# Kernel optimization log

Hardware: AMD Instinct MI355X
Metric: run time of the kernel (lower is better)

The kernel has to match this reference:

```python
import jax, jax.numpy as jnp
import numpy as np

L = 4          # num_layers
D = 512        # gconv_dim == tlayer_dim
HG, CG = 8, 64 # gconv heads, head dim (D//8)
HT, CT = 4, 128  # tlayer heads, head dim
FF = 4 * D
G, NPG = 128, 256
N = G * NPG
E = N * 16
AF, AV = 9, 64   # atom features / vocab
BF, BV = 3, 8    # bond features / vocab
OUT = 128
SCALE = 0.02


def setup_inputs() -> dict:
    key = jax.random.key(0)
    ks = iter(jax.random.split(key, 64))
    rn = lambda shape: (jax.random.normal(next(ks), shape, dtype=jnp.float32) * SCALE)
    inp = {}
    # float params (stacked over layers)
    inp['atom_emb'] = rn((AF, AV, D))
    inp['bond_emb'] = rn((BF, BV, D))
    for nm in ['gq_w', 'gk_w', 'gv_w', 'ge_w', 'gskip_w', 'mid_w']:
        inp[nm] = rn((L, D, D))
    for nm in ['gq_b', 'gk_b', 'gv_b', 'gskip_b', 'mid_b']:
        inp[nm] = rn((L, D))
    inp['mid_g'] = jnp.ones((L, D), jnp.float32)
    inp['mid_bt'] = jnp.zeros((L, D), jnp.float32)
    for nm in ['tq_w', 'tk_w', 'tv_w', 'to_w']:
        inp[nm] = rn((L, D, D))
    for nm in ['tq_b', 'tk_b', 'tv_b', 'to_b']:
        inp[nm] = rn((L, D))
    inp['ln1_g'] = jnp.ones((L, D), jnp.float32)
    inp['ln1_b'] = jnp.zeros((L, D), jnp.float32)
    inp['f1_w'] = rn((L, D, FF))
    inp['f1_b'] = rn((L, FF))
    inp['f2_w'] = rn((L, FF, D))
    inp['f2_b'] = rn((L, D))
    inp['ln2_g'] = jnp.ones((L, D), jnp.float32)
    inp['ln2_b'] = jnp.zeros((L, D), jnp.float32)
    inp['out_w'] = rn((D, OUT))
    inp['out_b'] = rn((OUT,))
    # int inputs
    inp['x'] = jax.random.randint(next(ks), (N, AF), 0, AV, dtype=jnp.int32)
    inp['edge_attr'] = jax.random.randint(next(ks), (E, BF), 0, BV, dtype=jnp.int32)
    # intra-graph edges: random offsets within each graph
    gid = jax.random.randint(next(ks), (E,), 0, G, dtype=jnp.int32)
    src = gid * NPG + jax.random.randint(next(ks), (E,), 0, NPG, dtype=jnp.int32)
    dst = gid * NPG + jax.random.randint(next(ks), (E,), 0, NPG, dtype=jnp.int32)
    inp['edge_index'] = jnp.stack([src, dst])
    inp['batch'] = jnp.repeat(jnp.arange(G, dtype=jnp.int32), NPG)
    return inp


def _ln(x, g, b, eps=1e-5):
    mu = x.mean(-1, keepdims=True)
    var = ((x - mu) ** 2).mean(-1, keepdims=True)
    return (x - mu) * jax.lax.rsqrt(var + eps) * g + b


def _forward(atom_emb, bond_emb, gq_w, gq_b, gk_w, gk_b, gv_w, gv_b, ge_w,
             gskip_w, gskip_b, mid_w, mid_b, mid_g, mid_bt,
             tq_w, tq_b, tk_w, tk_b, tv_w, tv_b, to_w, to_b,
             ln1_g, ln1_b, f1_w, f1_b, f2_w, f2_b, ln2_g, ln2_b,
             out_w, out_b, x, edge_index, edge_attr, batch):
    # encoders: sum of per-feature embeddings (OGB AtomEncoder/BondEncoder)
    h = atom_emb[jnp.arange(AF)[None, :], x].sum(1)          # [N, D]
    e_attr = bond_emb[jnp.arange(BF)[None, :], edge_attr].sum(1)  # [E, D]
    src, dst = edge_index[0], edge_index[1]

    for i in range(L):
        # --- TransformerConv (PyG): edge-conditioned multi-head graph attention
        q = (h @ gq_w[i] + gq_b[i]).reshape(N, HG, CG)
        k = (h @ gk_w[i] + gk_b[i]).reshape(N, HG, CG)
        v = (h @ gv_w[i] + gv_b[i]).reshape(N, HG, CG)
        ee = (e_attr @ ge_w[i]).reshape(E, HG, CG)           # lin_edge (no bias)
        ke = k[src] + ee
        ve = v[src] + ee
        logits = (q[dst] * ke).sum(-1) / np.sqrt(CG)          # [E, HG]
        m = jax.ops.segment_max(logits, dst, num_segments=N)
        p = jnp.exp(logits - m[dst])
        denom = jax.ops.segment_sum(p, dst, num_segments=N) + 1e-16
        alpha = p / denom[dst]
        agg = jax.ops.segment_sum(alpha[..., None] * ve, dst, num_segments=N)
        h = agg.reshape(N, D) + h @ gskip_w[i] + gskip_b[i]   # root skip
        # --- middle Linear + LayerNorm + ReLU
        h = jax.nn.relu(_ln(h @ mid_w[i] + mid_b[i], mid_g[i], mid_bt[i]))

    xg = h.reshape(G, NPG, D)
    for i in range(L):
        # --- transformer encoder layer, dense attention within each graph
        q = (xg @ tq_w[i] + tq_b[i]).reshape(G, NPG, HT, CT)
        k = (xg @ tk_w[i] + tk_b[i]).reshape(G, NPG, HT, CT)
        v = (xg @ tv_w[i] + tv_b[i]).reshape(G, NPG, HT, CT)
        attn = jax.nn.softmax(jnp.einsum('gqhc,gkhc->ghqk', q, k) / np.sqrt(CT), axis=-1)
        o = jnp.einsum('ghqk,gkhc->gqhc', attn, v).reshape(G, NPG, D)
        xg = _ln(xg + (o @ to_w[i] + to_b[i]), ln1_g[i], ln1_b[i])
        ff = jax.nn.relu(xg @ f1_w[i] + f1_b[i]) @ f2_w[i] + f2_b[i]
        xg = _ln(xg + ff, ln2_g[i], ln2_b[i])

    # mean readout over nodes per graph (segment mean via batch)
    hflat = xg.reshape(N, D)
    cnt = jax.ops.segment_sum(jnp.ones((N,), hflat.dtype), batch, num_segments=G)
    pooled = jax.ops.segment_sum(hflat, batch, num_segments=G) / cnt[:, None]
    return pooled @ out_w + out_b                              # [G, OUT]


def reference(atom_emb, bond_emb, gq_w, gq_b, gk_w, gk_b, gv_w, gv_b, ge_w,
              gskip_w, gskip_b, mid_w, mid_b, mid_g, mid_bt,
              tq_w, tq_b, tk_w, tk_b, tv_w, tv_b, to_w, to_b,
              ln1_g, ln1_b, f1_w, f1_b, f2_w, f2_b, ln2_g, ln2_b,
              out_w, out_b, x, edge_index, edge_attr, batch):
    return _forward(atom_emb, bond_emb, gq_w, gq_b, gk_w, gk_b, gv_w, gv_b, ge_w,
                    gskip_w, gskip_b, mid_w, mid_b, mid_g, mid_bt,
                    tq_w, tq_b, tk_w, tk_b, tv_w, tv_b, to_w, to_b,
                    ln1_g, ln1_b, f1_w, f1_b, f2_w, f2_b, ln2_g, ln2_b,
                    out_w, out_b, x, edge_index, edge_attr, batch)
```

## Files before the change

### kernel.cpp

```cpp
#include <hip/hip_runtime.h>
#include <hip/hip_bf16.h>
#include <math.h>

#define N_NODES 32768
#define DIM     512
#define NE      524288
#define NL      4
#define NG      128
#define NPG_    256
#define HG_     8
#define CG_     64
#define HT_     4
#define CT_     128
#define FF_     2048
#define AF_     9
#define AV_     64
#define BV_     8
#define OUTD    128

typedef unsigned short u16;
typedef __attribute__((ext_vector_type(8))) short bhalf8;
typedef __attribute__((ext_vector_type(4))) float floatx4;
typedef __attribute__((ext_vector_type(8))) unsigned short u16x8;
typedef __attribute__((ext_vector_type(4))) unsigned short u16x4;

__device__ __forceinline__ u16 f2bf(float f) {
  union { float f; unsigned u; } x; x.f = f;
  unsigned r = x.u + 0x7fffu + ((x.u >> 16) & 1u);
  return (u16)(r >> 16);
}
__device__ __forceinline__ float bf2f(u16 u) {
  union { unsigned u; float f; } x; x.u = ((unsigned)u) << 16; return x.f;
}

#define GL2LDS(gp, lp) __builtin_amdgcn_global_load_lds( \
    (const __attribute__((address_space(1))) unsigned int*)(gp), \
    (__attribute__((address_space(3))) unsigned int*)(lp), 16, 0, 0)

__global__ __launch_bounds__(128) void atom_enc_kernel(
    const float* __restrict__ emb, const int* __restrict__ x, u16* __restrict__ hb) {
  int n = blockIdx.x;
  int d4 = threadIdx.x;
  const int* xr = x + n * AF_;
  float4 acc = {0.f, 0.f, 0.f, 0.f};
#pragma unroll
  for (int f = 0; f < AF_; ++f) {
    int idx = xr[f];
    const float4 v = *(const float4*)&emb[((size_t)(f * AV_ + idx)) * DIM + 4 * d4];
    acc.x += v.x; acc.y += v.y; acc.z += v.z; acc.w += v.w;
  }
  u16x4 o;
  o[0] = f2bf(acc.x); o[1] = f2bf(acc.y); o[2] = f2bf(acc.z); o[3] = f2bf(acc.w);
  *(u16x4*)&hb[(size_t)n * DIM + 4 * d4] = o;
}

__global__ __launch_bounds__(512) void bemb_proj_kernel(
    const float* __restrict__ bond_emb, const float* __restrict__ gew, u16* __restrict__ tab) {
  int r = blockIdx.x;
  int d = threadIdx.x;
  const float* a = bond_emb + (size_t)r * DIM;
  float acc = 0.f;
#pragma unroll 8
  for (int kx = 0; kx < DIM; ++kx) acc += a[kx] * gew[(size_t)kx * DIM + d];
  tab[(size_t)r * DIM + d] = f2bf(acc);
}

__global__ __launch_bounds__(256) void wcvt_kernel(
    const float* __restrict__ W, u16* __restrict__ Wt, int K, int N) {
  __shared__ float t[32][33];
  const size_t mo = (size_t)blockIdx.z * K * N;
  int k0 = blockIdx.y * 32, n0 = blockIdx.x * 32;
  int tx = threadIdx.x & 31, ty = threadIdx.x >> 5;
#pragma unroll
  for (int i = 0; i < 32; i += 8)
    t[ty + i][tx] = W[mo + (size_t)(k0 + ty + i) * N + n0 + tx];
  __syncthreads();
#pragma unroll
  for (int i = 0; i < 32; i += 8)
    Wt[mo + (size_t)(n0 + ty + i) * K + k0 + tx] = f2bf(t[tx][ty + i]);
}

__global__ __launch_bounds__(256) void gemm_mfma_kernel(
    const u16* __restrict__ A, const u16* __restrict__ Bt,
    const float* __restrict__ bias, float* __restrict__ Cf, u16* __restrict__ Cb,
    int K, int Nout, int relu, int bf16out, int vtout) {
  __shared__ __align__(16) u16 As[4096];
  __shared__ __align__(16) u16 Bs[4096];
  const int tid = threadIdx.x;
  const int wave = tid >> 6, lane = tid & 63;
  const int bm = blockIdx.y * 128, bn = blockIdx.x * 128;
  const int wr = wave >> 1, wc = wave & 1;

  const size_t rowA = (size_t)bm + (tid >> 2);
  const size_t rowB = (size_t)bn + (tid >> 2);
  const int gofs = (tid & 3) * 8;
  const u16* pA = A + rowA * K + gofs;
  const u16* pB = Bt + rowB * K + gofs;
  u16* lA0 = &As[wave * 512];
  u16* lB0 = &Bs[wave * 512];
  const size_t skip64 = (size_t)64 * K;

  floatx4 acc[4][4] = {};
  const int r = lane & 15, kg = lane >> 4;
  const int aoff = (wr * 64 + r) * 32 + kg * 8;
  const int boff = (wc * 64 + r) * 32 + kg * 8;

  for (int k0 = 0; k0 < K; k0 += 32) {
    GL2LDS(pA + k0, lA0);
    GL2LDS(pA + skip64 + k0, lA0 + 2048);
    GL2LDS(pB + k0, lB0);
    GL2LDS(pB + skip64 + k0, lB0 + 2048);
    __syncthreads();
    bhalf8 af[4], bg[4];
#pragma unroll
    for (int mi = 0; mi < 4; ++mi) af[mi] = *(const bhalf8*)&As[aoff + mi * 512];
#pragma unroll
    for (int ni = 0; ni < 4; ++ni) bg[ni] = *(const bhalf8*)&Bs[boff + ni * 512];
#pragma unroll
    for (int mi = 0; mi < 4; ++mi)
#pragma unroll
      for (int ni = 0; ni < 4; ++ni)
        acc[mi][ni] = __builtin_amdgcn_mfma_f32_16x16x32_bf16(af[mi], bg[ni], acc[mi][ni], 0, 0, 0);
    __syncthreads();
  }

  const int rb = (lane >> 4) * 4;
  const int cc = lane & 15;
#pragma unroll
  for (int mi = 0; mi < 4; ++mi) {
#pragma unroll
    for (int ni = 0; ni < 4; ++ni) {
      int gr0 = bm + wr * 64 + mi * 16 + rb;
      int gc = bn + wc * 64 + ni * 16 + cc;
      float bv = bias[gc];
#pragma unroll
      for (int reg = 0; reg < 4; ++reg) {
        int gr = gr0 + reg;
        float v = acc[mi][ni][reg] + bv;
        if (relu) v = fmaxf(v, 0.f);
        if (vtout)        Cb[((size_t)(gr >> 8) * DIM + gc) * NPG_ + (gr & 255)] = f2bf(v);
        else if (bf16out) Cb[(size_t)gr * Nout + gc] = f2bf(v);
        else              Cf[(size_t)gr * Nout + gc] = v;
      }
    }
  }
}

__global__ __launch_bounds__(256) void attn_s_mfma_kernel(
    const u16* __restrict__ q, const u16* __restrict__ k, u16* __restrict__ S, int zbase) {
  __shared__ __align__(16) u16 As[4096];
  __shared__ __align__(16) u16 Bs[4096];
  const int tid = threadIdx.x;
  const int wave = tid >> 6, lane = tid & 63;
  const int zl = blockIdx.z, z = zbase + zl, g = z >> 2, hh = z & 3;
  const int bm = blockIdx.y * 128, bn = blockIdx.x * 128;
  const int wr = wave >> 1, wc = wave & 1;
  const u16* qg = q + (size_t)g * NPG_ * DIM + hh * CT_;
  const u16* kg2 = k + (size_t)g * NPG_ * DIM + hh * CT_;
  const u16* pA = qg + (size_t)(bm + (tid >> 2)) * DIM + (tid & 3) * 8;
  const u16* pB = kg2 + (size_t)(bn + (tid >> 2)) * DIM + (tid & 3) * 8;
  u16* lA0 = &As[wave * 512];
  u16* lB0 = &Bs[wave * 512];
  const size_t skip64 = (size_t)64 * DIM;
  floatx4 acc[4][4] = {};
  const int r = lane & 15, kg_ = lane >> 4;
  const int aoff = (wr * 64 + r) * 32 + kg_ * 8;
  const int boff = (wc * 64 + r) * 32 + kg_ * 8;
  for (int k0 = 0; k0 < CT_; k0 += 32) {
    GL2LDS(pA + k0, lA0);
    GL2LDS(pA + skip64 + k0, lA0 + 2048);
    GL2LDS(pB + k0, lB0);
    GL2LDS(pB + skip64 + k0, lB0 + 2048);
    __syncthreads();
    bhalf8 af[4], bg[4];
#pragma unroll
    for (int mi = 0; mi < 4; ++mi) af[mi] = *(const bhalf8*)&As[aoff + mi * 512];
#pragma unroll
    for (int ni = 0; ni < 4; ++ni) bg[ni] = *(const bhalf8*)&Bs[boff + ni * 512];
#pragma unroll
    for (int mi = 0; mi < 4; ++mi)
#pragma unroll
      for (int ni = 0; ni < 4; ++ni)
        acc[mi][ni] = __builtin_amdgcn_mfma_f32_16x16x32_bf16(af[mi], bg[ni], acc[mi][ni], 0, 0, 0);
    __syncthreads();
  }
  const float sc = 0.08838834764831845f;
  u16* C = S + (size_t)zl * NPG_ * NPG_;
  const int rb = (lane >> 4) * 4, cc = lane & 15;
#pragma unroll
  for (int mi = 0; mi < 4; ++mi)
#pragma unroll
    for (int ni = 0; ni < 4; ++ni) {
      int gr = bm + wr * 64 + mi * 16 + rb;
      int gc = bn + wc * 64 + ni * 16 + cc;
#pragma unroll
      for (int reg = 0; reg < 4; ++reg)
        C[(size_t)(gr + reg) * NPG_ + gc] = f2bf(acc[mi][ni][reg] * sc);
    }
}

__global__ __launch_bounds__(256) void softmax256_kernel(u16* __restrict__ SP) {
  size_t row = (size_t)blockIdx.x * 4 + (threadIdx.x >> 6);
  int lane = threadIdx.x & 63;
  u16* r = SP + row * NPG_;
  u16x4 v = *(u16x4*)&r[lane * 4];
  float x0 = bf2f(v[0]), x1 = bf2f(v[1]), x2 = bf2f(v[2]), x3 = bf2f(v[3]);
  float m = fmaxf(fmaxf(x0, x1), fmaxf(x2, x3));
#pragma unroll
  for (int off = 32; off; off >>= 1) m = fmaxf(m, __shfl_xor(m, off));
  x0 = expf(x0 - m); x1 = expf(x1 - m); x2 = expf(x2 - m); x3 = expf(x3 - m);
  float s = x0 + x1 + x2 + x3;
#pragma unroll
  for (int off = 32; off; off >>= 1) s += __shfl_xor(s, off);
  float inv = 1.0f / s;
  u16x4 o;
  o[0] = f2bf(x0 * inv); o[1] = f2bf(x1 * inv);
  o[2] = f2bf(x2 * inv); o[3] = f2bf(x3 * inv);
  *(u16x4*)&r[lane * 4] = o;
}

__global__ __launch_bounds__(256) void attn_o_mfma_kernel(
    const u16* __restrict__ P, const u16* __restrict__ vt, u16* __restrict__ O, int zbase) {
  __shared__ __align__(16) u16 As[4096];
  __shared__ __align__(16) u16 Bs[4096];
  const int tid = threadIdx.x;
  const int wave = tid >> 6, lane = tid & 63;
  const int zl = blockIdx.z, z = zbase + zl, g = z >> 2, hh = z & 3;
  const int bm = blockIdx.y * 128;
  const int wr = wave >> 1, wc = wave & 1;
  const u16* A = P + (size_t)zl * NPG_ * NPG_;
  const u16* Bt = vt + ((size_t)g * DIM + hh * CT_) * NPG_;
  const u16* pA = A + (size_t)(bm + (tid >> 2)) * NPG_ + (tid & 3) * 8;
  const u16* pB = Bt + (size_t)(tid >> 2) * NPG_ + (tid & 3) * 8;
  u16* lA0 = &As[wave * 512];
  u16* lB0 = &Bs[wave * 512];
  const size_t skip64 = (size_t)64 * NPG_;
  floatx4 acc[4][4] = {};
  const int r = lane & 15, kg_ = lane >> 4;
  const int aoff = (wr * 64 + r) * 32 + kg_ * 8;
  const int boff = (wc * 64 + r) * 32 + kg_ * 8;
  for (int k0 = 0; k0 < NPG_; k0 += 32) {
    GL2LDS(pA + k0, lA0);
    GL2LDS(pA + skip64 + k0, lA0 + 2048);
    GL2LDS(pB + k0, lB0);
    GL2LDS(pB + skip64 + k0, lB0 + 2048);
    __syncthreads();
    bhalf8 af[4], bg[4];
#pragma unroll
    for (int mi = 0; mi < 4; ++mi) af[mi] = *(const bhalf8*)&As[aoff + mi * 512];
#pragma unroll
    for (int ni = 0; ni < 4; ++ni) bg[ni] = *(const bhalf8*)&Bs[boff + ni * 512];
#pragma unroll
    for (int mi = 0; mi < 4; ++mi)
#pragma unroll
      for (int ni = 0; ni < 4; ++ni)
        acc[mi][ni] = __builtin_amdgcn_mfma_f32_16x16x32_bf16(af[mi], bg[ni], acc[mi][ni], 0, 0, 0);
    __syncthreads();
  }
  u16* C = O + ((size_t)g * NPG_) * DIM + hh * CT_;
  const int rb = (lane >> 4) * 4, cc = lane & 15;
#pragma unroll
  for (int mi = 0; mi < 4; ++mi)
#pragma unroll
    for (int ni = 0; ni < 4; ++ni) {
      int gr = bm + wr * 64 + mi * 16 + rb;
      int gc = wc * 64 + ni * 16 + cc;
#pragma unroll
      for (int reg = 0; reg < 4; ++reg)
        C[(size_t)(gr + reg) * DIM + gc] = f2bf(acc[mi][ni][reg]);
    }
}

__global__ __launch_bounds__(256) void gemm_bias_kernel(
    const float* __restrict__ A, const float* __restrict__ W,
    const float* __restrict__ bias, float* __restrict__ C,
    int M, int K, int Nout, int relu) {
  __shared__ float As[16][65];
  __shared__ float Bs[16][64];
  const int bm = blockIdx.y * 64;
  const int bn = blockIdx.x * 64;
  const int tid = threadIdx.x;
  const int tx = tid & 15, ty = tid >> 4;
  float acc[4][4] = {};
  for (int k0 = 0; k0 < K; k0 += 16) {
    {
      int row = tid >> 2;
      int kq = (tid & 3) << 2;
      float4 a = *(const float4*)&A[(size_t)(bm + row) * K + k0 + kq];
      As[kq + 0][row] = a.x; As[kq + 1][row] = a.y; As[kq + 2][row] = a.z; As[kq + 3][row] = a.w;
    }
    {
      int krow = tid >> 4;
      int cq = (tid & 15) << 2;
      *(float4*)&Bs[krow][cq] = *(const float4*)&W[(size_t)(k0 + krow) * Nout + bn + cq];
    }
    __syncthreads();
#pragma unroll
    for (int kk = 0; kk < 16; ++kk) {
      float a[4];
#pragma unroll
      for (int i = 0; i < 4; ++i) a[i] = As[kk][ty * 4 + i];
      float4 b4 = *(const float4*)&Bs[kk][tx * 4];
      float b[4] = {b4.x, b4.y, b4.z, b4.w};
#pragma unroll
      for (int i = 0; i < 4; ++i)
#pragma unroll
        for (int j = 0; j < 4; ++j) acc[i][j] = fmaf(a[i], b[j], acc[i][j]);
    }
    __syncthreads();
  }
  float4 bv = *(const float4*)&bias[bn + tx * 4];
#pragma unroll
  for (int i = 0; i < 4; ++i) {
    int row = bm + ty * 4 + i;
    float4 o;
    o.x = acc[i][0] + bv.x; o.y = acc[i][1] + bv.y;
    o.z = acc[i][2] + bv.z; o.w = acc[i][3] + bv.w;
    if (relu) {
      o.x = fmaxf(o.x, 0.f); o.y = fmaxf(o.y, 0.f);
      o.z = fmaxf(o.z, 0.f); o.w = fmaxf(o.w, 0.f);
    }
    *(float4*)&C[(size_t)row * Nout + bn + tx * 4] = o;
  }
}

__global__ __launch_bounds__(256) void deg_count_kernel(const int* __restrict__ ei, int* __restrict__ deg) {
  int e = blockIdx.x * 256 + threadIdx.x;
  atomicAdd(&deg[ei[NE + e]], 1);
}

__global__ __launch_bounds__(1024) void scan_kernel(const int* __restrict__ deg, int* __restrict__ rp) {
  __shared__ int sums[1024];
  int t = threadIdx.x;
  int base = t * 32;
  int local[32];
  int s = 0;
#pragma unroll
  for (int i = 0; i < 32; ++i) { local[i] = s; s += deg[base + i]; }
  sums[t] = s;
  __syncthreads();
  for (int off = 1; off < 1024; off <<= 1) {
    int other = (t >= off) ? sums[t - off] : 0;
    __syncthreads();
    sums[t] += other;
    __syncthreads();
  }
  int chunk_off = sums[t] - s;
#pragma unroll
  for (int i = 0; i < 32; ++i) rp[base + i] = chunk_off + local[i];
  if (t == 1023) rp[N_NODES] = sums[1023];
}

__global__ __launch_bounds__(256) void scatter_kernel(
    const int* __restrict__ ei, const int* __restrict__ rp,
    int* __restrict__ cur, int* __restrict__ csr) {
  int e = blockIdx.x * 256 + threadIdx.x;
  int d = ei[NE + e];
  int pos = atomicAdd(&cur[d], 1);
  csr[rp[d] + pos] = e;
}

__global__ __launch_bounds__(256) void edge_logits_kernel(
    const u16* __restrict__ q, const u16* __restrict__ k, const u16* __restrict__ tab,
    const int* __restrict__ ei, const int* __restrict__ ea, float* __restrict__ logits) {
  int e = blockIdx.x * 4 + (threadIdx.x >> 6);
  int lane = threadIdx.x & 63;
  int src = ei[e], dst = ei[NE + e];
  int a0 = ea[e * 3], a1 = ea[e * 3 + 1], a2 = ea[e * 3 + 2];
  const u16x8 qv = *(const u16x8*)&q[(size_t)dst * DIM + lane * 8];
  const u16x8 kv = *(const u16x8*)&k[(size_t)src * DIM + lane * 8];
  const size_t to = (size_t)lane * 8;
  const u16x8 e0 = *(const u16x8*)&tab[(size_t)a0 * DIM + to];
  const u16x8 e1 = *(const u16x8*)&tab[(size_t)(8 + a1) * DIM + to];
  const u16x8 e2 = *(const u16x8*)&tab[(size_t)(16 + a2) * DIM + to];
  float acc = 0.f;
#pragma unroll
  for (int j = 0; j < 8; ++j) {
    float ee = bf2f(e0[j]) + bf2f(e1[j]) + bf2f(e2[j]);
    acc += bf2f(qv[j]) * (bf2f(kv[j]) + ee);
  }
  acc += __shfl_xor(acc, 1);
  acc += __shfl_xor(acc, 2);
  acc += __shfl_xor(acc, 4);
  if ((lane & 7) == 0) logits[(size_t)e * HG_ + (lane >> 3)] = acc * 0.125f;
}

#define CHUNK 128
__global__ __launch_bounds__(512) void edge_agg_kernel(
    const u16* __restrict__ v, const u16* __restrict__ tab, const float* __restrict__ logits,
    const float* __restrict__ skip, const int* __restrict__ ei, const int* __restrict__ ea,
    const int* __restrict__ rp, const int* __restrict__ csr, u16* __restrict__ hnew) {
  int n = blockIdx.x;
  int d = threadIdx.x;
  int hh = d >> 6;
  int start = rp[n];
  int deg = rp[n + 1] - start;
  __shared__ int s_src[CHUNK];
  __shared__ int s_ea[CHUNK];
  __shared__ int s_eid[CHUNK];
  __shared__ float s_l[CHUNK * HG_];
  float runmax = -3.0e38f, denom = 0.f, accum = 0.f;
  for (int c0 = 0; c0 < deg; c0 += CHUNK) {
    int cnt = min(CHUNK, deg - c0);
    __syncthreads();
    if (d < cnt) {
      int eid = csr[start + c0 + d];
      s_eid[d] = eid;
      s_src[d] = ei[eid];
      s_ea[d] = ea[eid * 3] | (ea[eid * 3 + 1] << 8) | (ea[eid * 3 + 2] << 16);
    }
    __syncthreads();
    for (int j = d; j < cnt * HG_; j += 512)
      s_l[j] = logits[(size_t)s_eid[j >> 3] * HG_ + (j & 7)];
    __syncthreads();
    float cmax = -3.0e38f;
    for (int j = 0; j < cnt; ++j) cmax = fmaxf(cmax, s_l[j * HG_ + hh]);
    float nm = fmaxf(runmax, cmax);
    if (nm > runmax) {
      float rr = expf(runmax - nm);
      denom *= rr; accum *= rr; runmax = nm;
    }
    for (int j = 0; j < cnt; ++j) {
      float p = expf(s_l[j * HG_ + hh] - runmax);
      int srcn = s_src[j];
      int eap = s_ea[j];
      float ee = bf2f(tab[(size_t)(eap & 0xff) * DIM + d])
               + bf2f(tab[(size_t)(8 + ((eap >> 8) & 0xff)) * DIM + d])
               + bf2f(tab[(size_t)(16 + (eap >> 16)) * DIM + d]);
      float ve = bf2f(v[(size_t)srcn * DIM + d]) + ee;
      denom += p;
      accum += p * ve;
    }
  }
  size_t o = (size_t)n * DIM + d;
  hnew[o] = f2bf(accum / (denom + 1e-16f) + skip[o]);
}

__global__ __launch_bounds__(256) void ln_kernel(
    const float* __restrict__ in, const u16* __restrict__ resid,
    const float* __restrict__ g, const float* __restrict__ b,
    u16* __restrict__ outb, int relu) {
  int row = blockIdx.x * 4 + (threadIdx.x >> 6);
  int lane = threadIdx.x & 63;
  size_t base = (size_t)row * DIM + lane * 8;
  float x[8];
  {
    float4 v0 = *(const float4*)&in[base];
    float4 v1 = *(const float4*)&in[base + 4];
    x[0] = v0.x; x[1] = v0.y; x[2] = v0.z; x[3] = v0.w;
    x[4] = v1.x; x[5] = v1.y; x[6] = v1.z; x[7] = v1.w;
  }
  if (resid) {
    u16x8 rv = *(const u16x8*)&resid[base];
#pragma unroll
    for (int i = 0; i < 8; ++i) x[i] += bf2f(rv[i]);
  }
  float s = 0.f;
#pragma unroll
  for (int i = 0; i < 8; ++i) s += x[i];
#pragma unroll
  for (int off = 32; off; off >>= 1) s += __shfl_xor(s, off);
  float mu = s * (1.0f / DIM);
  float vs = 0.f;
#pragma unroll
  for (int i = 0; i < 8; ++i) { float t = x[i] - mu; vs += t * t; }
#pragma unroll
  for (int off = 32; off; off >>= 1) vs += __shfl_xor(vs, off);
  float rstd = 1.0f / sqrtf(vs * (1.0f / DIM) + 1e-5f);
  float4 g0 = *(const float4*)&g[lane * 8];
  float4 g1 = *(const float4*)&g[lane * 8 + 4];
  float4 b0 = *(const float4*)&b[lane * 8];
  float4 b1 = *(const float4*)&b[lane * 8 + 4];
  float gg[8] = {g0.x, g0.y, g0.z, g0.w, g1.x, g1.y, g1.z, g1.w};
  float bb[8] = {b0.x, b0.y, b0.z, b0.w, b1.x, b1.y, b1.z, b1.w};
  u16x8 ob;
#pragma unroll
  for (int i = 0; i < 8; ++i) {
    float y = (x[i] - mu) * rstd * gg[i] + bb[i];
    if (relu) y = fmaxf(y, 0.f);
    ob[i] = f2bf(y);
  }
  *(u16x8*)&outb[base] = ob;
}

__global__ __launch_bounds__(512) void pool_kernel(const u16* __restrict__ xg, float* __restrict__ pooled) {
  int g = blockIdx.x;
  int d = threadIdx.x;
  float acc = 0.f;
  for (int p = 0; p < NPG_; ++p) acc += bf2f(xg[((size_t)g * NPG_ + p) * DIM + d]);
  pooled[(size_t)g * DIM + d] = acc * (1.0f / NPG_);
}

extern "C" void kernel_launch(void* const* d_in, const int* in_sizes, int n_in,
                              void* d_out, int out_size, void* d_ws, size_t ws_size,
                              hipStream_t stream) {
  const float* atom_emb = (const float*)d_in[0];
  const float* bond_emb = (const float*)d_in[1];
  const float* gq_w = (const float*)d_in[2];
  const float* gk_w = (const float*)d_in[3];
  const float* gv_w = (const float*)d_in[4];
  const float* ge_w = (const float*)d_in[5];
  const float* gskip_w = (const float*)d_in[6];
  const float* mid_w = (const float*)d_in[7];
  const float* gq_b = (const float*)d_in[8];
  const float* gk_b = (const float*)d_in[9];
  const float* gv_b = (const float*)d_in[10];
  const float* gskip_b = (const float*)d_in[11];
  const float* mid_b = (const float*)d_in[12];
  const float* mid_g = (const float*)d_in[13];
  const float* mid_bt = (const float*)d_in[14];
  const float* tq_w = (const float*)d_in[15];
  const float* tk_w = (const float*)d_in[16];
  const float* tv_w = (const float*)d_in[17];
  const float* to_w = (const float*)d_in[18];
  const float* tq_b = (const float*)d_in[19];
  const float* tk_b = (const float*)d_in[20];
  const float* tv_b = (const float*)d_in[21];
  const float* to_b = (const float*)d_in[22];
  const float* ln1_g = (const float*)d_in[23];
  const float* ln1_b = (const float*)d_in[24];
  const float* f1_w = (const float*)d_in[25];
  const float* f1_b = (const float*)d_in[26];
  const float* f2_w = (const float*)d_in[27];
  const float* f2_b = (const float*)d_in[28];
  const float* ln2_g = (const float*)d_in[29];
  const float* ln2_b = (const float*)d_in[30];
  const float* out_w = (const float*)d_in[31];
  const float* out_b = (const float*)d_in[32];
  const int* x = (const int*)d_in[33];
  const int* ea = (const int*)d_in[34];
  const int* ei = (const int*)d_in[35];

  char* wbase = (char*)d_ws;
  size_t woff = 0;
  auto ALLOC = [&](size_t bytes) -> void* {
    void* r = wbase + woff;
    woff += (bytes + 255) & ~(size_t)255;
    return r;
  };
  const size_t ND = (size_t)N_NODES * DIM * sizeof(float);
  const size_t NDH = (size_t)N_NODES * DIM * sizeof(u16);
  u16*   wt     = (u16*)ALLOC((size_t)17825792 * sizeof(u16));
  u16*   hb     = (u16*)ALLOC(NDH);
  u16*   Abuf   = (u16*)ALLOC(NDH);
  u16*   Bbuf   = (u16*)ALLOC(NDH);
  u16*   Cbuf   = (u16*)ALLOC(NDH);
  float* E      = (float*)ALLOC(ND);
  u16*   U      = (u16*)ALLOC((size_t)16777216);
  u16*   tab    = (u16*)ALLOC(24 * DIM * sizeof(u16));
  float* pooled = (float*)ALLOC((size_t)NG * DIM * sizeof(float));
  int* deg      = (int*)ALLOC(N_NODES * sizeof(int));
  int* cur      = (int*)ALLOC(N_NODES * sizeof(int));
  int* rp       = (int*)ALLOC((N_NODES + 1) * sizeof(int));
  int* csr      = (int*)ALLOC((size_t)NE * sizeof(int));
  (void)ws_size; (void)in_sizes; (void)n_in; (void)out_size;

  const size_t DD = (size_t)DIM * DIM;
  const size_t DD4 = 4 * DD;
  u16* gqT = wt;            u16* gkT = wt + DD4;      u16* gvT = wt + 2 * DD4;
  u16* gskipT = wt + 3*DD4; u16* midT = wt + 4 * DD4;
  u16* tqT = wt + 5 * DD4;  u16* tkT = wt + 6 * DD4;  u16* tvT = wt + 7 * DD4;
  u16* toT = wt + 8 * DD4;
  u16* f1T = wt + 9 * DD4;
  u16* f2T = f1T + (size_t)4 * DIM * FF_;

  auto wcvt = [&](const float* W, u16* Wt, int K, int N, int L2) {
    dim3 grid(N / 32, K / 32, L2);
    wcvt_kernel<<<grid, 256, 0, stream>>>(W, Wt, K, N);
  };
  auto mgemm = [&](const u16* A_, const u16* Bt_, const float* bias_,
                   float* Cf_, u16* Cb_, int M_, int K_, int Nout_,
                   int relu_, int bf16o_, int vtout_) {
    dim3 grid(Nout_ / 128, M_ / 128);
    gemm_mfma_kernel<<<grid, 256, 0, stream>>>(A_, Bt_, bias_, Cf_, Cb_, K_, Nout_, relu_, bf16o_, vtout_);
  };

  wcvt(gq_w, gqT, DIM, DIM, 4);   wcvt(gk_w, gkT, DIM, DIM, 4);
  wcvt(gv_w, gvT, DIM, DIM, 4);   wcvt(gskip_w, gskipT, DIM, DIM, 4);
  wcvt(mid_w, midT, DIM, DIM, 4);
  wcvt(tq_w, tqT, DIM, DIM, 4);   wcvt(tk_w, tkT, DIM, DIM, 4);
  wcvt(tv_w, tvT, DIM, DIM, 4);   wcvt(to_w, toT, DIM, DIM, 4);
  wcvt(f1_w, f1T, DIM, FF_, 4);   wcvt(f2_w, f2T, FF_, DIM, 4);

  hipMemsetAsync(deg, 0, N_NODES * sizeof(int), stream);
  hipMemsetAsync(cur, 0, N_NODES * sizeof(int), stream);
  deg_count_kernel<<<NE / 256, 256, 0, stream>>>(ei, deg);
  scan_kernel<<<1, 1024, 0, stream>>>(deg, rp);
  scatter_kernel<<<NE / 256, 256, 0, stream>>>(ei, rp, cur, csr);

  atom_enc_kernel<<<N_NODES, 128, 0, stream>>>(atom_emb, x, hb);

  for (int i = 0; i < NL; ++i) {
    bemb_proj_kernel<<<24, 512, 0, stream>>>(bond_emb, ge_w + i * DD, tab);
    mgemm(hb, gqT + i * DD, gq_b + i * DIM, nullptr, Abuf, N_NODES, DIM, DIM, 0, 1, 0);
    mgemm(hb, gkT + i * DD, gk_b + i * DIM, nullptr, Bbuf, N_NODES, DIM, DIM, 0, 1, 0);
    mgemm(hb, gvT + i * DD, gv_b + i * DIM, nullptr, Cbuf, N_NODES, DIM, DIM, 0, 1, 0);
    mgemm(hb, gskipT + i * DD, gskip_b + i * DIM, E, nullptr, N_NODES, DIM, DIM, 0, 0, 0);
    edge_logits_kernel<<<NE / 4, 256, 0, stream>>>(Abuf, Bbuf, tab, ei, ea, (float*)U);
    edge_agg_kernel<<<N_NODES, 512, 0, stream>>>(Cbuf, tab, (float*)U, E, ei, ea, rp, csr, Abuf);
    mgemm(Abuf, midT + i * DD, mid_b + i * DIM, E, nullptr, N_NODES, DIM, DIM, 0, 0, 0);
    ln_kernel<<<N_NODES / 4, 256, 0, stream>>>(E, nullptr, mid_g + i * DIM, mid_bt + i * DIM, hb, 1);
  }

  for (int i = 0; i < NL; ++i) {
    mgemm(hb, tqT + i * DD, tq_b + i * DIM, nullptr, Abuf, N_NODES, DIM, DIM, 0, 1, 0);
    mgemm(hb, tkT + i * DD, tk_b + i * DIM, nullptr, Bbuf, N_NODES, DIM, DIM, 0, 1, 0);
    mgemm(hb, tvT + i * DD, tv_b + i * DIM, nullptr, Cbuf, N_NODES, DIM, DIM, 0, 1, 1);
    for (int rnd = 0; rnd < 4; ++rnd) {
      attn_s_mfma_kernel<<<dim3(2, 2, 128), 256, 0, stream>>>(Abuf, Bbuf, U, rnd * 128);
      softmax256_kernel<<<(128 * NPG_) / 4, 256, 0, stream>>>(U);
      attn_o_mfma_kernel<<<dim3(1, 2, 128), 256, 0, stream>>>(U, Cbuf, Abuf, rnd * 128);
    }
    mgemm(Abuf, toT + i * DD, to_b + i * DIM, E, nullptr, N_NODES, DIM, DIM, 0, 0, 0);
    ln_kernel<<<N_NODES / 4, 256, 0, stream>>>(E, hb, ln1_g + i * DIM, ln1_b + i * DIM, hb, 0);
    for (int c = 0; c < 4; ++c) {
      mgemm(hb + (size_t)c * 8192 * DIM, f1T + (size_t)i * DIM * FF_, f1_b + i * FF_,
            nullptr, Abuf, 8192, DIM, FF_, 1, 1, 0);
      mgemm(Abuf, f2T + (size_t)i * FF_ * DIM, f2_b + i * DIM,
            E + (size_t)c * 8192 * DIM, nullptr, 8192, FF_, DIM, 0, 0, 0);
    }
    ln_kernel<<<N_NODES / 4, 256, 0, stream>>>(E, hb, ln2_g + i * DIM, ln2_b + i * DIM, hb, 0);
  }

  pool_kernel<<<NG, 512, 0, stream>>>(hb, pooled);
  gemm_bias_kernel<<<dim3(OUTD / 64, NG / 64), 256, 0, stream>>>(pooled, out_w, out_b, (float*)d_out, NG, DIM, OUTD, 0);
}
```

Measured before the change: 5.974 ms.

## Factor edge-embedding term out of aggregation via per-bond-value weight sums

The edge aggregation kernel no longer gathers three bond-table rows per edge per channel. It accumulates softmax weights per (bond feature value, head) in shared memory with atomics, then applies the 24 table rows once at the end. The online softmax is restructured to use a wave-level max and shared rescale factors. The bond projection kernel is also split across K and column blocks for more parallelism. This adds shared atomics and extra barriers per chunk.

```diff
diff --git a/kernel.cpp b/kernel.cpp
--- a/kernel.cpp
+++ b/kernel.cpp
@@ -56,13 +56,24 @@
 
 __global__ __launch_bounds__(512) void bemb_proj_kernel(
     const float* __restrict__ bond_emb, const float* __restrict__ gew, u16* __restrict__ tab) {
+  __shared__ float red[8][64];
   int r = blockIdx.x;
-  int d = threadIdx.x;
-  const float* a = bond_emb + (size_t)r * DIM;
+  int col = (threadIdx.x & 63) + blockIdx.y * 64;
+  int kp = threadIdx.x >> 6;
+  const float* a = bond_emb + (size_t)r * DIM + kp * 64;
+  const float* w = gew + (size_t)kp * 64 * DIM + col;
   float acc = 0.f;
 #pragma unroll 8
-  for (int kx = 0; kx < DIM; ++kx) acc += a[kx] * gew[(size_t)kx * DIM + d];
-  tab[(size_t)r * DIM + d] = f2bf(acc);
+  for (int kx = 0; kx < 64; ++kx)
+    acc += a[kx] * w[(size_t)kx * DIM];
+  red[kp][threadIdx.x & 63] = acc;
+  __syncthreads();
+  if (threadIdx.x < 64) {
+    float s = 0.f;
+#pragma unroll
+    for (int p = 0; p < 8; ++p) s += red[p][threadIdx.x];
+    tab[(size_t)r * DIM + col] = f2bf(s);
+  }
 }
 
 __global__ __launch_bounds__(256) void wcvt_kernel(
@@ -393,13 +404,19 @@
   int n = blockIdx.x;
   int d = threadIdx.x;
   int hh = d >> 6;
+  int lane = d & 63;
   int start = rp[n];
   int deg = rp[n + 1] - start;
+  __shared__ int s_eid[CHUNK];
   __shared__ int s_src[CHUNK];
   __shared__ int s_ea[CHUNK];
-  __shared__ int s_eid[CHUNK];
-  __shared__ float s_l[CHUNK * HG_];
-  float runmax = -3.0e38f, denom = 0.f, accum = 0.f;
+  __shared__ float s_p[CHUNK * HG_];
+  __shared__ float s_w[24 * HG_];
+  __shared__ float s_max[HG_];
+  __shared__ float s_resc[HG_];
+  if (d < 24 * HG_) s_w[d] = 0.f;
+  if (d < HG_) s_max[d] = -3.0e38f;
+  float accum = 0.f, den = 0.f;
   for (int c0 = 0; c0 < deg; c0 += CHUNK) {
     int cnt = min(CHUNK, deg - c0);
     __syncthreads();
@@ -410,30 +427,48 @@
       s_ea[d] = ea[eid * 3] | (ea[eid * 3 + 1] << 8) | (ea[eid * 3 + 2] << 16);
     }
     __syncthreads();
-    for (int j = d; j < cnt * HG_; j += 512)
-      s_l[j] = logits[(size_t)s_eid[j >> 3] * HG_ + (j & 7)];
-    __syncthreads();
-    float cmax = -3.0e38f;
-    for (int j = 0; j < cnt; ++j) cmax = fmaxf(cmax, s_l[j * HG_ + hh]);
-    float nm = fmaxf(runmax, cmax);
-    if (nm > runmax) {
-      float rr = expf(runmax - nm);
-      denom *= rr; accum *= rr; runmax = nm;
-    }
+    for (int jh = d; jh < cnt * HG_; jh += 512)
+      s_p[jh] = logits[(size_t)s_eid[jh >> 3] * HG_ + (jh & 7)];
+    __syncthreads();
+    float cm = -3.0e38f;
+    for (int j = lane; j < cnt; j += 64)
+      cm = fmaxf(cm, s_p[j * HG_ + hh]);
+#pragma unroll
+    for (int off = 32; off; off >>= 1) cm = fmaxf(cm, __shfl_xor(cm, off));
+    if (lane == 0) {
+      float om = s_max[hh];
+      float nm = fmaxf(om, cm);
+      s_resc[hh] = (nm > om) ? expf(om - nm) : 1.0f;
+      s_max[hh] = nm;
+    }
+    __syncthreads();
+    float rsc = s_resc[hh];
+    accum *= rsc;
+    den *= rsc;
+    if (d < 24 * HG_) s_w[d] *= s_resc[d & 7];
+    __syncthreads();
+    for (int jh = d; jh < cnt * HG_; jh += 512) {
+      int h2 = jh & 7;
+      float p = expf(s_p[jh] - s_max[h2]);
+      s_p[jh] = p;
+      int eap = s_ea[jh >> 3];
+      atomicAdd(&s_w[(eap & 0xff) * HG_ + h2], p);
+      atomicAdd(&s_w[(8 + ((eap >> 8) & 0xff)) * HG_ + h2], p);
+      atomicAdd(&s_w[(16 + (eap >> 16)) * HG_ + h2], p);
+    }
+    __syncthreads();
     for (int j = 0; j < cnt; ++j) {
-      float p = expf(s_l[j * HG_ + hh] - runmax);
-      int srcn = s_src[j];
-      int eap = s_ea[j];
-      float ee = bf2f(tab[(size_t)(eap & 0xff) * DIM + d])
-               + bf2f(tab[(size_t)(8 + ((eap >> 8) & 0xff)) * DIM + d])
-               + bf2f(tab[(size_t)(16 + (eap >> 16)) * DIM + d]);
-      float ve = bf2f(v[(size_t)srcn * DIM + d]) + ee;
-      denom += p;
-      accum += p * ve;
-    }
-  }
+      float p = s_p[j * HG_ + hh];
+      den += p;
+      accum = fmaf(p, bf2f(v[(size_t)s_src[j] * DIM + d]), accum);
+    }
+  }
+  __syncthreads();
+#pragma unroll
+  for (int r2 = 0; r2 < 24; ++r2)
+    accum = fmaf(s_w[r2 * HG_ + hh], bf2f(tab[(size_t)r2 * DIM + d]), accum);
   size_t o = (size_t)n * DIM + d;
-  hnew[o] = f2bf(accum / (denom + 1e-16f) + skip[o]);
+  hnew[o] = f2bf(accum / (den + 1e-16f) + skip[o]);
 }
 
 __global__ __launch_bounds__(256) void ln_kernel(
@@ -591,7 +626,7 @@
   atom_enc_kernel<<<N_NODES, 128, 0, stream>>>(atom_emb, x, hb);
 
   for (int i = 0; i < NL; ++i) {
-    bemb_proj_kernel<<<24, 512, 0, stream>>>(bond_emb, ge_w + i * DD, tab);
+    bemb_proj_kernel<<<dim3(24, 8), 512, 0, stream>>>(bond_emb, ge_w + i * DD, tab);
     mgemm(hb, gqT + i * DD, gq_b + i * DIM, nullptr, Abuf, N_NODES, DIM, DIM, 0, 1, 0);
     mgemm(hb, gkT + i * DD, gk_b + i * DIM, nullptr, Bbuf, N_NODES, DIM, DIM, 0, 1, 0);
     mgemm(hb, gvT + i * DD, gv_b + i * DIM, nullptr, Cbuf, N_NODES, DIM, DIM, 0, 1, 0);
```

New measurement: 5.624 ms. 1.06x faster.
